# Performance work log

Hardware: AMD Instinct MI355X
Metric: run time of the kernel (lower is better)

## Reference

```python
import jax, jax.numpy as jnp
import numpy as np

N_ATOMS = 50000
N_EDGES = 800000
NODE_DIM = 64
EDGE_DIM = 64
FULL_DIM = 2 * NODE_DIM + EDGE_DIM
BN_EPS = 1e-5


def setup_inputs() -> dict:
    key = jax.random.key(0)
    ks = jax.random.split(key, 8)
    atom_features = jax.random.normal(ks[0], (N_ATOMS, NODE_DIM), dtype=jnp.float32)
    edge_features = jax.random.normal(ks[1], (N_EDGES, EDGE_DIM), dtype=jnp.float32)
    edge_indices = jax.random.randint(ks[2], (N_EDGES, 2), 0, N_ATOMS, dtype=jnp.int64)
    lim = 1.0 / np.sqrt(FULL_DIM)
    W_filter = jax.random.uniform(ks[3], (NODE_DIM, FULL_DIM), jnp.float32, -lim, lim)
    b_filter = jax.random.uniform(ks[4], (NODE_DIM,), jnp.float32, -lim, lim)
    W_core = jax.random.uniform(ks[5], (NODE_DIM, FULL_DIM), jnp.float32, -lim, lim)
    b_core = jax.random.uniform(ks[6], (NODE_DIM,), jnp.float32, -lim, lim)
    gamma_filter = jnp.ones((NODE_DIM,), jnp.float32)
    beta_filter = jnp.zeros((NODE_DIM,), jnp.float32)
    gamma_core = jnp.ones((NODE_DIM,), jnp.float32)
    beta_core = jnp.zeros((NODE_DIM,), jnp.float32)
    return {
        "atom_features": atom_features,
        "edge_features": edge_features,
        "W_filter": W_filter, "b_filter": b_filter,
        "gamma_filter": gamma_filter, "beta_filter": beta_filter,
        "W_core": W_core, "b_core": b_core,
        "gamma_core": gamma_core, "beta_core": beta_core,
        "edge_indices": edge_indices,
    }


def _batchnorm(x, gamma, beta):
    # training-mode BN over the edge axis (biased variance, as torch uses for normalization)
    mean = jnp.mean(x, axis=0)
    var = jnp.mean(jnp.square(x - mean), axis=0)
    return (x - mean) * jax.lax.rsqrt(var + BN_EPS) * gamma + beta


def reference(atom_features, edge_features, W_filter, b_filter, gamma_filter,
              beta_filter, W_core, b_core, gamma_core, beta_core, edge_indices):
    src = edge_indices[:, 0]
    dst = edge_indices[:, 1]
    # z_ij: [E, 2*node_dim + edge_dim]
    z = jnp.concatenate([atom_features[dst], atom_features[src], edge_features], axis=1)
    signal = jax.nn.softplus(_batchnorm(z @ W_core.T + b_core, gamma_core, beta_core))
    gate = jax.nn.sigmoid(_batchnorm(z @ W_filter.T + b_filter, gamma_filter, beta_filter))
    message = gate * signal  # [E, node_dim]
    nbr_sumed = jax.ops.segment_sum(message, dst, num_segments=atom_features.shape[0])
    return atom_features + nbr_sumed
```

## Files before the change

kernel.cpp:

```cpp
#include <hip/hip_runtime.h>
#include <hip/hip_bf16.h>
#include <math.h>

#define N_ATOMS   50000
#define N_EDGES   800000
#define KDIM      192
#define BN_EPS    1e-5f

#define TILE_E     64
#define TPB        5
#define NTILES     (N_EDGES / TILE_E)
#define GRID1      (NTILES / TPB)
#define STAT_SLOTS 32
#define ZSTRIDE    200
#define NSCANBLK   ((N_ATOMS + 255) / 256)

typedef __attribute__((ext_vector_type(8))) __bf16 bf16x8;
typedef __attribute__((ext_vector_type(4))) float  f32x4;
typedef __attribute__((ext_vector_type(4))) unsigned short u16x4;

__device__ __forceinline__ ushort f2bf(float f) {
    union { float f; unsigned u; } v; v.f = f;
    unsigned u = v.u;
    return (ushort)((u + 0x7FFFu + ((u >> 16) & 1u)) >> 16);
}
__device__ __forceinline__ float bf2f(unsigned hi16) {
    union { unsigned u; float f; } v; v.u = hi16 << 16; return v.f;
}
__device__ __forceinline__ float msgf(unsigned pv, float sc_c, float sh_c,
                                      float sc_f, float sh_f) {
    float pc = fmaf(bf2f(pv & 0xFFFFu), sc_c, sh_c);
    float pf = fmaf(bf2f(pv >> 16),     sc_f, sh_f);
    float sp = fmaxf(pc, 0.f) + __logf(1.f + __expf(-fabsf(pc)));
    float sg = 1.f / (1.f + __expf(-pf));
    return sp * sg;
}

__device__ __forceinline__ void gather_issue(
    const float* __restrict__ atom, const float* __restrict__ edgef,
    const int* __restrict__ eidx, int tilebase, int tid, f32x4* v)
{
    const int er = tid >> 4, f4 = tid & 15;
#pragma unroll
    for (int it = 0; it < 12; ++it) {
        const int seg = it >> 2;
        const int e   = (it & 3) * 16 + er;
        const float* srcp;
        if (seg == 0)      srcp = atom  + (size_t)eidx[2 * (tilebase + e) + 1] * 64;
        else if (seg == 1) srcp = atom  + (size_t)eidx[2 * (tilebase + e)] * 64;
        else               srcp = edgef + (size_t)(tilebase + e) * 64;
        v[it] = *(const f32x4*)(srcp + f4 * 4);
    }
}

__device__ __forceinline__ void gather_commit(const f32x4* v, ushort* zl, int tid)
{
    const int er = tid >> 4, f4 = tid & 15;
#pragma unroll
    for (int it = 0; it < 12; ++it) {
        const int seg = it >> 2;
        const int e   = (it & 3) * 16 + er;
        u16x4 b;
        b.x = f2bf(v[it].x); b.y = f2bf(v[it].y);
        b.z = f2bf(v[it].z); b.w = f2bf(v[it].w);
        *(u16x4*)&zl[e * ZSTRIDE + seg * 64 + f4 * 4] = b;
    }
}

__global__ __launch_bounds__(256) void gemm_stats_store(
    const float* __restrict__ atom, const float* __restrict__ edgef,
    const ushort* __restrict__ Wb, const int* __restrict__ eidx,
    const unsigned* __restrict__ perm,
    float* __restrict__ stat_partial, unsigned* __restrict__ ws_pre,
    int do_store)
{
    __shared__ __align__(16) ushort zbuf[2][TILE_E * ZSTRIDE];
    __shared__ unsigned perml[TPB * TILE_E];
    const int tid  = threadIdx.x;
    const int lane = tid & 63, wave = tid >> 6;
    const int ch = wave >> 1, rp = wave & 1;
    const int row = lane & 15, quad = lane >> 4;

    const int t0 = blockIdx.x * TPB;
    for (int i = tid; i < TPB * TILE_E; i += 256)
        perml[i] = perm[t0 * TILE_E + i];

    bf16x8 bfr[2][2][6];
#pragma unroll
    for (int m = 0; m < 2; ++m)
#pragma unroll
        for (int nt = 0; nt < 2; ++nt)
#pragma unroll
            for (int ks = 0; ks < 6; ++ks)
                bfr[m][nt][ks] = *(const bf16x8*)&Wb[
                    (size_t)(m * 64 + ch * 32 + nt * 16 + row) * KDIM + ks * 32 + quad * 8];

    float s[2][2] = {{0.f, 0.f}, {0.f, 0.f}};
    float q[2][2] = {{0.f, 0.f}, {0.f, 0.f}};

    f32x4 pre[12];
    gather_issue(atom, edgef, eidx, t0 * TILE_E, tid, pre);

    for (int tt = 0; tt < TPB; ++tt) {
        ushort* zl = zbuf[tt & 1];
        gather_commit(pre, zl, tid);
        __syncthreads();
        if (tt + 1 < TPB)
            gather_issue(atom, edgef, eidx, (t0 + tt + 1) * TILE_E, tid, pre);

#pragma unroll
        for (int ett = 0; ett < 2; ++ett) {
            const ushort* zb = zl + ((2 * rp + ett) * 16 + row) * ZSTRIDE;
            bf16x8 a[6];
#pragma unroll
            for (int ks = 0; ks < 6; ++ks)
                a[ks] = *(const bf16x8*)&zb[ks * 32 + quad * 8];
            f32x4 acc[2][2];
#pragma unroll
            for (int m = 0; m < 2; ++m)
#pragma unroll
                for (int nt = 0; nt < 2; ++nt)
                    acc[m][nt] = (f32x4){0.f, 0.f, 0.f, 0.f};
#pragma unroll
            for (int ks = 0; ks < 6; ++ks)
#pragma unroll
                for (int m = 0; m < 2; ++m)
#pragma unroll
                    for (int nt = 0; nt < 2; ++nt)
                        acc[m][nt] = __builtin_amdgcn_mfma_f32_16x16x32_bf16(
                            a[ks], bfr[m][nt][ks], acc[m][nt], 0, 0, 0);
#pragma unroll
            for (int nt = 0; nt < 2; ++nt) {
                const int c = ch * 32 + nt * 16 + row;
#pragma unroll
                for (int r = 0; r < 4; ++r) {
                    float vc = acc[0][nt][r], vf = acc[1][nt][r];
                    s[0][nt] += vc; q[0][nt] += vc * vc;
                    s[1][nt] += vf; q[1][nt] += vf * vf;
                    if (do_store) {
                        const int eloc = (2 * rp + ett) * 16 + quad * 4 + r;
                        const unsigned pos = perml[tt * TILE_E + eloc];
                        unsigned pack = (unsigned)f2bf(vc) | ((unsigned)f2bf(vf) << 16);
                        ws_pre[(size_t)pos * 64 + c] = pack;
                    }
                }
            }
        }
    }

    float* slot = stat_partial + (size_t)(blockIdx.x & (STAT_SLOTS - 1)) * 256;
#pragma unroll
    for (int m = 0; m < 2; ++m)
#pragma unroll
        for (int nt = 0; nt < 2; ++nt) {
            float sv = s[m][nt], qv = q[m][nt];
            sv += __shfl_xor(sv, 16, 64); sv += __shfl_xor(sv, 32, 64);
            qv += __shfl_xor(qv, 16, 64); qv += __shfl_xor(qv, 32, 64);
            if (lane < 16) {
                int c = ch * 32 + nt * 16 + lane;
                atomicAdd(slot + m * 128 + c, sv);
                atomicAdd(slot + m * 128 + 64 + c, qv);
            }
        }
}

__global__ void finalize_stats(const float* __restrict__ stat_partial,
                               const float* __restrict__ gc, const float* __restrict__ btc,
                               const float* __restrict__ gf, const float* __restrict__ btf,
                               float* __restrict__ params)
{
    int t = threadIdx.x;
    bool isf = t >= 64;
    int j = t & 63;
    float s = 0.f, q = 0.f;
    for (int slot = 0; slot < STAT_SLOTS; slot++) {
        const float* sp = stat_partial + (size_t)slot * 256 + (isf ? 128 : 0);
        s += sp[j];
        q += sp[64 + j];
    }
    float mean = s / (float)N_EDGES;
    float var  = q / (float)N_EDGES - mean * mean;
    float inv  = rsqrtf(var + BN_EPS);
    float gamma = isf ? gf[j] : gc[j];
    float beta  = isf ? btf[j] : btc[j];
    float scale = gamma * inv;
    float shift = beta - mean * scale;
    params[t]       = scale;
    params[128 + t] = shift;
}

__global__ __launch_bounds__(256) void convert_weights(
    const float* __restrict__ Wc, const float* __restrict__ Wf,
    ushort* __restrict__ Wb)
{
    int i = blockIdx.x * 256 + threadIdx.x;
    float v = (i < 64 * KDIM) ? Wc[i] : Wf[i - 64 * KDIM];
    Wb[i] = f2bf(v);
}

__global__ __launch_bounds__(256) void hist_dst(const int* __restrict__ eidx,
                                                unsigned* __restrict__ counts)
{
    int e = blockIdx.x * 256 + threadIdx.x;
    atomicAdd(&counts[eidx[2 * e + 1]], 1u);
}

__global__ __launch_bounds__(256) void scan_a(const unsigned* __restrict__ counts,
                                              unsigned* __restrict__ row_start,
                                              unsigned* __restrict__ blksum)
{
    __shared__ unsigned sh[256];
    const int tid = threadIdx.x;
    const int i = blockIdx.x * 256 + tid;
    unsigned v = (i < N_ATOMS) ? counts[i] : 0u;
    sh[tid] = v;
    __syncthreads();
    for (int off = 1; off < 256; off <<= 1) {
        unsigned t = (tid >= off) ? sh[tid - off] : 0u;
        __syncthreads();
        sh[tid] += t;
        __syncthreads();
    }
    if (i < N_ATOMS) row_start[i] = sh[tid] - v;
    if (tid == 255) blksum[blockIdx.x] = sh[tid];
}

__global__ void scan_b(unsigned* __restrict__ blksum)
{
    __shared__ unsigned sh[256];
    const int tid = threadIdx.x;
    unsigned v = (tid < NSCANBLK) ? blksum[tid] : 0u;
    sh[tid] = v;
    __syncthreads();
    for (int off = 1; off < 256; off <<= 1) {
        unsigned t = (tid >= off) ? sh[tid - off] : 0u;
        __syncthreads();
        sh[tid] += t;
        __syncthreads();
    }
    if (tid < NSCANBLK) blksum[tid] = sh[tid] - v;
}

__global__ __launch_bounds__(256) void init_cursor(unsigned* __restrict__ row_start,
                                                   const unsigned* __restrict__ blksum,
                                                   unsigned* __restrict__ cursors)
{
    int i = blockIdx.x * 256 + threadIdx.x;
    if (i < N_ATOMS) {
        unsigned base = row_start[i] + blksum[i >> 8];
        row_start[i] = base;
        cursors[i]   = base;
    }
    if (i == 0) row_start[N_ATOMS] = N_EDGES;
}

__global__ __launch_bounds__(256) void fill_perm(const int* __restrict__ eidx,
                                                 unsigned* __restrict__ cursors,
                                                 unsigned* __restrict__ perm)
{
    int e = blockIdx.x * 256 + threadIdx.x;
    int d = eidx[2 * e + 1];
    perm[e] = atomicAdd(&cursors[d], 1u);
}

__global__ __launch_bounds__(256) void bn_act_reduce(
    const unsigned* __restrict__ ws_pre, const unsigned* __restrict__ row_start,
    const float* __restrict__ atom, const float* __restrict__ params,
    float* __restrict__ out)
{
    const int lane = threadIdx.x & 63;
    const int a    = blockIdx.x * 4 + (threadIdx.x >> 6);

    const float sc_c = params[lane],      sh_c = params[128 + lane];
    const float sc_f = params[64 + lane], sh_f = params[192 + lane];

    const unsigned jb = row_start[a];
    const unsigned n  = row_start[a + 1] - jb;
    const unsigned* base = ws_pre + (size_t)jb * 64 + lane;

    float acc = 0.f;
    unsigned k = 0;
    for (; k + 8 <= n; k += 8) {
        unsigned p[8];
#pragma unroll
        for (int u = 0; u < 8; ++u) p[u] = base[(size_t)(k + u) * 64];
#pragma unroll
        for (int u = 0; u < 8; ++u) acc += msgf(p[u], sc_c, sh_c, sc_f, sh_f);
    }
    for (; k < n; ++k) acc += msgf(base[(size_t)k * 64], sc_c, sh_c, sc_f, sh_f);

    out[(size_t)a * 64 + lane] = atom[(size_t)a * 64 + lane] + acc;
}

__global__ __launch_bounds__(256) void copy_out(const f32x4* __restrict__ src,
                                                f32x4* __restrict__ dst)
{
    int i = blockIdx.x * blockDim.x + threadIdx.x;
    dst[i] = src[i];
}

__global__ __launch_bounds__(256) void apply_scatter_fb(
    const float* __restrict__ atom, const float* __restrict__ edgef,
    const ushort* __restrict__ Wb, const int* __restrict__ eidx,
    const float* __restrict__ params, float* __restrict__ out)
{
    __shared__ __align__(16) ushort zl[TILE_E * ZSTRIDE];
    const int tid  = threadIdx.x;
    const int lane = tid & 63, wave = tid >> 6;
    const int ch = wave >> 1, rp = wave & 1;
    const int row = lane & 15, quad = lane >> 4;

    bf16x8 bfr[2][2][6];
#pragma unroll
    for (int m = 0; m < 2; ++m)
#pragma unroll
        for (int nt = 0; nt < 2; ++nt)
#pragma unroll
            for (int ks = 0; ks < 6; ++ks)
                bfr[m][nt][ks] = *(const bf16x8*)&Wb[
                    (size_t)(m * 64 + ch * 32 + nt * 16 + row) * KDIM + ks * 32 + quad * 8];

    float scc[2], shc[2], scf[2], shf[2];
#pragma unroll
    for (int nt = 0; nt < 2; ++nt) {
        int c = ch * 32 + nt * 16 + row;
        scc[nt] = params[c];        shc[nt] = params[128 + c];
        scf[nt] = params[64 + c];   shf[nt] = params[192 + c];
    }

    const int t0 = blockIdx.x * TPB;
    for (int tt = 0; tt < TPB; ++tt) {
        const int tilebase = (t0 + tt) * TILE_E;
        f32x4 pre[12];
        gather_issue(atom, edgef, eidx, tilebase, tid, pre);
        __syncthreads();
        gather_commit(pre, zl, tid);
        __syncthreads();
#pragma unroll
        for (int ett = 0; ett < 2; ++ett) {
            const ushort* zb = zl + ((2 * rp + ett) * 16 + row) * ZSTRIDE;
            bf16x8 a[6];
#pragma unroll
            for (int ks = 0; ks < 6; ++ks)
                a[ks] = *(const bf16x8*)&zb[ks * 32 + quad * 8];
            f32x4 acc[2][2];
#pragma unroll
            for (int m = 0; m < 2; ++m)
#pragma unroll
                for (int nt = 0; nt < 2; ++nt)
                    acc[m][nt] = (f32x4){0.f, 0.f, 0.f, 0.f};
#pragma unroll
            for (int ks = 0; ks < 6; ++ks)
#pragma unroll
                for (int m = 0; m < 2; ++m)
#pragma unroll
                    for (int nt = 0; nt < 2; ++nt)
                        acc[m][nt] = __builtin_amdgcn_mfma_f32_16x16x32_bf16(
                            a[ks], bfr[m][nt][ks], acc[m][nt], 0, 0, 0);
#pragma unroll
            for (int nt = 0; nt < 2; ++nt) {
                int c = ch * 32 + nt * 16 + row;
#pragma unroll
                for (int r = 0; r < 4; ++r) {
                    float pc = fmaf(acc[0][nt][r], scc[nt], shc[nt]);
                    float pf = fmaf(acc[1][nt][r], scf[nt], shf[nt]);
                    float sp = fmaxf(pc, 0.f) + __logf(1.f + __expf(-fabsf(pc)));
                    float sg = 1.f / (1.f + __expf(-pf));
                    int eloc = (2 * rp + ett) * 16 + quad * 4 + r;
                    int d = eidx[2 * (tilebase + eloc) + 1];
                    atomicAdd(out + (size_t)d * 64 + c, sp * sg);
                }
            }
        }
    }
}

extern "C" void kernel_launch(void* const* d_in, const int* in_sizes, int n_in,
                              void* d_out, int out_size, void* d_ws, size_t ws_size,
                              hipStream_t stream)
{
    const float* atom  = (const float*)d_in[0];
    const float* edgef = (const float*)d_in[1];
    const float* Wf    = (const float*)d_in[2];
    const float* gf    = (const float*)d_in[4];
    const float* btf   = (const float*)d_in[5];
    const float* Wc    = (const float*)d_in[6];
    const float* gc    = (const float*)d_in[8];
    const float* btc   = (const float*)d_in[9];
    const int*   eidx  = (const int*)d_in[10];
    float* out = (float*)d_out;

    unsigned* ws_pre       = (unsigned*)d_ws;
    float*    stat_partial = (float*)(ws_pre + (size_t)N_EDGES * 64);
    float*    params       = stat_partial + STAT_SLOTS * 256;
    ushort*   Wb           = (ushort*)(params + 256);
    unsigned* counts       = (unsigned*)(Wb + 2 * 64 * KDIM);
    unsigned* row_start    = counts + N_ATOMS;
    unsigned* blksum       = row_start + N_ATOMS + 1;
    unsigned* cursors      = blksum + 256;
    unsigned* perm         = cursors + N_ATOMS;

    const size_t need_full = (size_t)((char*)(perm + N_EDGES) - (char*)d_ws);
    const int full = (ws_size >= need_full) ? 1 : 0;

    (void)hipMemsetAsync(stat_partial, 0, STAT_SLOTS * 256 * sizeof(float), stream);
    convert_weights<<<(2 * 64 * KDIM) / 256, 256, 0, stream>>>(Wc, Wf, Wb);

    if (full) {
        (void)hipMemsetAsync(counts, 0, N_ATOMS * sizeof(unsigned), stream);
        hist_dst<<<N_EDGES / 256, 256, 0, stream>>>(eidx, counts);
        scan_a<<<NSCANBLK, 256, 0, stream>>>(counts, row_start, blksum);
        scan_b<<<1, 256, 0, stream>>>(blksum);
        init_cursor<<<NSCANBLK, 256, 0, stream>>>(row_start, blksum, cursors);
        fill_perm<<<N_EDGES / 256, 256, 0, stream>>>(eidx, cursors, perm);
        gemm_stats_store<<<GRID1, 256, 0, stream>>>(atom, edgef, Wb, eidx, perm,
                                                    stat_partial, ws_pre, 1);
        finalize_stats<<<1, 128, 0, stream>>>(stat_partial, gc, btc, gf, btf, params);
        bn_act_reduce<<<N_ATOMS / 4, 256, 0, stream>>>(ws_pre, row_start,
                                                       atom, params, out);
    } else {
        gemm_stats_store<<<GRID1, 256, 0, stream>>>(atom, edgef, Wb, eidx,
                                                    (unsigned*)counts ,
                                                    stat_partial, ws_pre, 0);
        finalize_stats<<<1, 128, 0, stream>>>(stat_partial, gc, btc, gf, btf, params);
        copy_out<<<(N_ATOMS * 64 / 4) / 256, 256, 0, stream>>>(
            (const f32x4*)atom, (f32x4*)out);
        apply_scatter_fb<<<GRID1, 256, 0, stream>>>(atom, edgef, Wb, eidx,
                                                    params, out);
    }
}
```

Before: 530.9 us.

## Replace tiled GEMM-stats kernel with persistent per-wave direct-gather variant

The GEMM+stats kernel is rewritten so that each wave independently processes 16-edge groups in a grid-stride persistent loop. It loads the A operand directly from global memory into registers and converts it to bf16 there, with no shared-memory staging and no per-tile __syncthreads. Weights are kept in LDS and read once per MFMA, and edge indices and permutation entries are prefetched two iterations ahead. The aim is to remove the LDS round-trip and the block barriers, at the cost of more LDS reads for B and a different occupancy profile.

```diff
diff --git a/kernel.cpp b/kernel.cpp
--- a/kernel.cpp
+++ b/kernel.cpp
@@ -15,9 +15,16 @@
 #define ZSTRIDE    200
 #define NSCANBLK   ((N_ATOMS + 255) / 256)
 
+#define NGROUPS   (N_EDGES / 16)
+#define GRID_DIR  768
+#define GSTRIDE   (GRID_DIR * 4)
+#define WLSTRIDE  200
+
 typedef __attribute__((ext_vector_type(8))) __bf16 bf16x8;
 typedef __attribute__((ext_vector_type(4))) float  f32x4;
 typedef __attribute__((ext_vector_type(4))) unsigned short u16x4;
+typedef __attribute__((ext_vector_type(8))) unsigned short u16x8;
+typedef __attribute__((ext_vector_type(4))) unsigned int   u32x4;
 
 __device__ __forceinline__ ushort f2bf(float f) {
     union { float f; unsigned u; } v; v.f = f;
@@ -34,6 +41,150 @@
     float sp = fmaxf(pc, 0.f) + __logf(1.f + __expf(-fabsf(pc)));
     float sg = 1.f / (1.f + __expf(-pf));
     return sp * sg;
+}
+
+__global__ __launch_bounds__(256, 3) void gemm_stats_direct(
+    const float* __restrict__ atom, const float* __restrict__ edgef,
+    const ushort* __restrict__ Wb, const int* __restrict__ eidx,
+    const unsigned* __restrict__ perm,
+    float* __restrict__ stat_partial, unsigned* __restrict__ ws_pre,
+    int do_store)
+{
+    __shared__ __align__(16) ushort Wl[128 * WLSTRIDE];
+    const int tid  = threadIdx.x;
+    const int lane = tid & 63;
+    const int r    = lane & 15;
+    const int q    = lane >> 4;
+
+    {
+        const int row = tid >> 1, half = tid & 1;
+        const ushort* srcW = Wb + (size_t)row * KDIM + half * 96;
+        ushort*       dstW = Wl + row * WLSTRIDE + half * 96;
+#pragma unroll
+        for (int j = 0; j < 12; ++j)
+            *(u16x8*)&dstW[j * 8] = *(const u16x8*)&srcW[j * 8];
+    }
+    __syncthreads();
+
+    const int wave  = tid >> 6;
+    const int wglob = blockIdx.x * 4 + wave;
+    const int NG    = (NGROUPS - wglob + GSTRIDE - 1) / GSTRIDE;
+
+    float s[2][4], qs[2][4];
+#pragma unroll
+    for (int m = 0; m < 2; ++m)
+#pragma unroll
+        for (int nt = 0; nt < 4; ++nt) { s[m][nt] = 0.f; qs[m][nt] = 0.f; }
+
+    int2  eA = {0, 0}, eB = {0, 0};
+    u32x4 pA = (u32x4){0, 0, 0, 0}, pB = (u32x4){0, 0, 0, 0};
+    f32x4 pre[12];
+
+    int g = wglob;
+    eA = *(const int2*)&eidx[2 * (g * 16 + r)];
+    if (do_store) pA = *(const u32x4*)&perm[g * 16 + q * 4];
+    if (NG >= 2) {
+        eB = *(const int2*)&eidx[2 * ((g + GSTRIDE) * 16 + r)];
+        if (do_store) pB = *(const u32x4*)&perm[(g + GSTRIDE) * 16 + q * 4];
+    }
+    {
+        const float* pd = atom  + (size_t)eA.y * 64;
+        const float* ps = atom  + (size_t)eA.x * 64;
+        const float* pe = edgef + ((size_t)g * 16 + r) * 64;
+#pragma unroll
+        for (int ks = 0; ks < 6; ++ks) {
+            const float* sp = (ks < 2) ? pd : (ks < 4) ? ps : pe;
+            const int col = (ks & 1) * 32 + q * 8;
+            pre[2 * ks]     = *(const f32x4*)(sp + col);
+            pre[2 * ks + 1] = *(const f32x4*)(sp + col + 4);
+        }
+    }
+
+    for (int i = 0; i < NG; ++i, g += GSTRIDE) {
+        bf16x8 a[6];
+#pragma unroll
+        for (int ks = 0; ks < 6; ++ks) {
+            union { u16x8 u; bf16x8 b; } t;
+#pragma unroll
+            for (int j = 0; j < 4; ++j) {
+                t.u[j]     = f2bf(pre[2 * ks][j]);
+                t.u[4 + j] = f2bf(pre[2 * ks + 1][j]);
+            }
+            a[ks] = t.b;
+        }
+
+        if (i + 1 < NG) {
+            const int gn = g + GSTRIDE;
+            const float* pd = atom  + (size_t)eB.y * 64;
+            const float* ps = atom  + (size_t)eB.x * 64;
+            const float* pe = edgef + ((size_t)gn * 16 + r) * 64;
+#pragma unroll
+            for (int ks = 0; ks < 6; ++ks) {
+                const float* sp = (ks < 2) ? pd : (ks < 4) ? ps : pe;
+                const int col = (ks & 1) * 32 + q * 8;
+                pre[2 * ks]     = *(const f32x4*)(sp + col);
+                pre[2 * ks + 1] = *(const f32x4*)(sp + col + 4);
+            }
+        }
+        int2  eC = {0, 0};
+        u32x4 pC = (u32x4){0, 0, 0, 0};
+        if (i + 2 < NG) {
+            const int g2 = g + 2 * GSTRIDE;
+            eC = *(const int2*)&eidx[2 * (g2 * 16 + r)];
+            if (do_store) pC = *(const u32x4*)&perm[g2 * 16 + q * 4];
+        }
+
+        f32x4 acc[2][4];
+#pragma unroll
+        for (int m = 0; m < 2; ++m)
+#pragma unroll
+            for (int nt = 0; nt < 4; ++nt)
+                acc[m][nt] = (f32x4){0.f, 0.f, 0.f, 0.f};
+#pragma unroll
+        for (int ks = 0; ks < 6; ++ks)
+#pragma unroll
+            for (int m = 0; m < 2; ++m)
+#pragma unroll
+                for (int nt = 0; nt < 4; ++nt) {
+                    bf16x8 b = *(const bf16x8*)&Wl[
+                        (m * 64 + nt * 16 + r) * WLSTRIDE + ks * 32 + q * 8];
+                    acc[m][nt] = __builtin_amdgcn_mfma_f32_16x16x32_bf16(
+                        a[ks], b, acc[m][nt], 0, 0, 0);
+                }
+
+#pragma unroll
+        for (int nt = 0; nt < 4; ++nt) {
+            const int c = nt * 16 + r;
+#pragma unroll
+            for (int rr = 0; rr < 4; ++rr) {
+                float vc = acc[0][nt][rr], vf = acc[1][nt][rr];
+                s[0][nt] += vc; qs[0][nt] += vc * vc;
+                s[1][nt] += vf; qs[1][nt] += vf * vf;
+                if (do_store) {
+                    const unsigned pos = pA[rr];
+                    unsigned pack = (unsigned)f2bf(vc) | ((unsigned)f2bf(vf) << 16);
+                    ws_pre[(size_t)pos * 64 + c] = pack;
+                }
+            }
+        }
+
+        eA = eB; eB = eC; pA = pB; pB = pC;
+    }
+
+    float* slot = stat_partial + (size_t)(blockIdx.x & (STAT_SLOTS - 1)) * 256;
+#pragma unroll
+    for (int m = 0; m < 2; ++m)
+#pragma unroll
+        for (int nt = 0; nt < 4; ++nt) {
+            float sv = s[m][nt], qv = qs[m][nt];
+            sv += __shfl_xor(sv, 16, 64); sv += __shfl_xor(sv, 32, 64);
+            qv += __shfl_xor(qv, 16, 64); qv += __shfl_xor(qv, 32, 64);
+            if (lane < 16) {
+                int c = nt * 16 + lane;
+                atomicAdd(slot + m * 128 + c, sv);
+                atomicAdd(slot + m * 128 + 64 + c, qv);
+            }
+        }
 }
 
 __device__ __forceinline__ void gather_issue(
@@ -65,103 +216,6 @@
         b.z = f2bf(v[it].z); b.w = f2bf(v[it].w);
         *(u16x4*)&zl[e * ZSTRIDE + seg * 64 + f4 * 4] = b;
     }
-}
-
-__global__ __launch_bounds__(256) void gemm_stats_store(
-    const float* __restrict__ atom, const float* __restrict__ edgef,
-    const ushort* __restrict__ Wb, const int* __restrict__ eidx,
-    const unsigned* __restrict__ perm,
-    float* __restrict__ stat_partial, unsigned* __restrict__ ws_pre,
-    int do_store)
-{
-    __shared__ __align__(16) ushort zbuf[2][TILE_E * ZSTRIDE];
-    __shared__ unsigned perml[TPB * TILE_E];
-    const int tid  = threadIdx.x;
-    const int lane = tid & 63, wave = tid >> 6;
-    const int ch = wave >> 1, rp = wave & 1;
-    const int row = lane & 15, quad = lane >> 4;
-
-    const int t0 = blockIdx.x * TPB;
-    for (int i = tid; i < TPB * TILE_E; i += 256)
-        perml[i] = perm[t0 * TILE_E + i];
-
-    bf16x8 bfr[2][2][6];
-#pragma unroll
-    for (int m = 0; m < 2; ++m)
-#pragma unroll
-        for (int nt = 0; nt < 2; ++nt)
-#pragma unroll
-            for (int ks = 0; ks < 6; ++ks)
-                bfr[m][nt][ks] = *(const bf16x8*)&Wb[
-                    (size_t)(m * 64 + ch * 32 + nt * 16 + row) * KDIM + ks * 32 + quad * 8];
-
-    float s[2][2] = {{0.f, 0.f}, {0.f, 0.f}};
-    float q[2][2] = {{0.f, 0.f}, {0.f, 0.f}};
-
-    f32x4 pre[12];
-    gather_issue(atom, edgef, eidx, t0 * TILE_E, tid, pre);
-
-    for (int tt = 0; tt < TPB; ++tt) {
-        ushort* zl = zbuf[tt & 1];
-        gather_commit(pre, zl, tid);
-        __syncthreads();
-        if (tt + 1 < TPB)
-            gather_issue(atom, edgef, eidx, (t0 + tt + 1) * TILE_E, tid, pre);
-
-#pragma unroll
-        for (int ett = 0; ett < 2; ++ett) {
-            const ushort* zb = zl + ((2 * rp + ett) * 16 + row) * ZSTRIDE;
-            bf16x8 a[6];
-#pragma unroll
-            for (int ks = 0; ks < 6; ++ks)
-                a[ks] = *(const bf16x8*)&zb[ks * 32 + quad * 8];
-            f32x4 acc[2][2];
-#pragma unroll
-            for (int m = 0; m < 2; ++m)
-#pragma unroll
-                for (int nt = 0; nt < 2; ++nt)
-                    acc[m][nt] = (f32x4){0.f, 0.f, 0.f, 0.f};
-#pragma unroll
-            for (int ks = 0; ks < 6; ++ks)
-#pragma unroll
-                for (int m = 0; m < 2; ++m)
-#pragma unroll
-                    for (int nt = 0; nt < 2; ++nt)
-                        acc[m][nt] = __builtin_amdgcn_mfma_f32_16x16x32_bf16(
-                            a[ks], bfr[m][nt][ks], acc[m][nt], 0, 0, 0);
-#pragma unroll
-            for (int nt = 0; nt < 2; ++nt) {
-                const int c = ch * 32 + nt * 16 + row;
-#pragma unroll
-                for (int r = 0; r < 4; ++r) {
-                    float vc = acc[0][nt][r], vf = acc[1][nt][r];
-                    s[0][nt] += vc; q[0][nt] += vc * vc;
-                    s[1][nt] += vf; q[1][nt] += vf * vf;
-                    if (do_store) {
-                        const int eloc = (2 * rp + ett) * 16 + quad * 4 + r;
-                        const unsigned pos = perml[tt * TILE_E + eloc];
-                        unsigned pack = (unsigned)f2bf(vc) | ((unsigned)f2bf(vf) << 16);
-                        ws_pre[(size_t)pos * 64 + c] = pack;
-                    }
-                }
-            }
-        }
-    }
-
-    float* slot = stat_partial + (size_t)(blockIdx.x & (STAT_SLOTS - 1)) * 256;
-#pragma unroll
-    for (int m = 0; m < 2; ++m)
-#pragma unroll
-        for (int nt = 0; nt < 2; ++nt) {
-            float sv = s[m][nt], qv = q[m][nt];
-            sv += __shfl_xor(sv, 16, 64); sv += __shfl_xor(sv, 32, 64);
-            qv += __shfl_xor(qv, 16, 64); qv += __shfl_xor(qv, 32, 64);
-            if (lane < 16) {
-                int c = ch * 32 + nt * 16 + lane;
-                atomicAdd(slot + m * 128 + c, sv);
-                atomicAdd(slot + m * 128 + 64 + c, qv);
-            }
-        }
 }
 
 __global__ void finalize_stats(const float* __restrict__ stat_partial,
@@ -413,15 +467,15 @@
         scan_b<<<1, 256, 0, stream>>>(blksum);
         init_cursor<<<NSCANBLK, 256, 0, stream>>>(row_start, blksum, cursors);
         fill_perm<<<N_EDGES / 256, 256, 0, stream>>>(eidx, cursors, perm);
-        gemm_stats_store<<<GRID1, 256, 0, stream>>>(atom, edgef, Wb, eidx, perm,
-                                                    stat_partial, ws_pre, 1);
+        gemm_stats_direct<<<GRID_DIR, 256, 0, stream>>>(atom, edgef, Wb, eidx, perm,
+                                                        stat_partial, ws_pre, 1);
         finalize_stats<<<1, 128, 0, stream>>>(stat_partial, gc, btc, gf, btf, params);
         bn_act_reduce<<<N_ATOMS / 4, 256, 0, stream>>>(ws_pre, row_start,
                                                        atom, params, out);
     } else {
-        gemm_stats_store<<<GRID1, 256, 0, stream>>>(atom, edgef, Wb, eidx,
-                                                    (unsigned*)counts ,
-                                                    stat_partial, ws_pre, 0);
+        gemm_stats_direct<<<GRID_DIR, 256, 0, stream>>>(atom, edgef, Wb, eidx,
+                                                        (const unsigned*)counts ,
+                                                        stat_partial, ws_pre, 0);
         finalize_stats<<<1, 128, 0, stream>>>(stat_partial, gc, btc, gf, btf, params);
         copy_out<<<(N_ATOMS * 64 / 4) / 256, 256, 0, stream>>>(
             (const f32x4*)atom, (f32x4*)out);
```

After: 864.5 us. 62.9% more time.

## Load edge features directly into MFMA registers, bypassing LDS staging

Applied to the files above, without the earlier changes.

Edge-feature rows are no longer copied through the shared-memory tile. Each wave now reads them straight from global memory in MFMA A-fragment layout and converts them to bf16 in registers. The LDS tile keeps only the two gathered atom segments, with a smaller row stride, which cuts LDS footprint and store traffic and lets the kernel declare a higher occupancy hint. In exchange, the edge loads are no longer prefetched a tile ahead, so global latency may be exposed inside the MFMA loop, and each lane does strided 32-byte reads.

```diff
diff --git a/kernel.cpp b/kernel.cpp
--- a/kernel.cpp
+++ b/kernel.cpp
@@ -13,11 +13,13 @@
 #define GRID1      (NTILES / TPB)
 #define STAT_SLOTS 32
 #define ZSTRIDE    200
+#define ZAST       136
 #define NSCANBLK   ((N_ATOMS + 255) / 256)
 
 typedef __attribute__((ext_vector_type(8))) __bf16 bf16x8;
 typedef __attribute__((ext_vector_type(4))) float  f32x4;
 typedef __attribute__((ext_vector_type(4))) unsigned short u16x4;
+typedef __attribute__((ext_vector_type(8))) unsigned short u16x8;
 
 __device__ __forceinline__ ushort f2bf(float f) {
     union { float f; unsigned u; } v; v.f = f;
@@ -34,6 +36,35 @@
     float sp = fmaxf(pc, 0.f) + __logf(1.f + __expf(-fabsf(pc)));
     float sg = 1.f / (1.f + __expf(-pf));
     return sp * sg;
+}
+
+__device__ __forceinline__ void gather_issue_a(
+    const float* __restrict__ atom, const int* __restrict__ eidx,
+    int tilebase, int tid, f32x4* v)
+{
+    const int er = tid >> 4, f4 = tid & 15;
+#pragma unroll
+    for (int it = 0; it < 8; ++it) {
+        const int seg = it >> 2;
+        const int e   = (it & 3) * 16 + er;
+        const float* srcp =
+            atom + (size_t)eidx[2 * (tilebase + e) + (seg == 0 ? 1 : 0)] * 64;
+        v[it] = *(const f32x4*)(srcp + f4 * 4);
+    }
+}
+
+__device__ __forceinline__ void gather_commit_a(const f32x4* v, ushort* zl, int tid)
+{
+    const int er = tid >> 4, f4 = tid & 15;
+#pragma unroll
+    for (int it = 0; it < 8; ++it) {
+        const int seg = it >> 2;
+        const int e   = (it & 3) * 16 + er;
+        u16x4 b;
+        b.x = f2bf(v[it].x); b.y = f2bf(v[it].y);
+        b.z = f2bf(v[it].z); b.w = f2bf(v[it].w);
+        *(u16x4*)&zl[e * ZAST + seg * 64 + f4 * 4] = b;
+    }
 }
 
 __device__ __forceinline__ void gather_issue(
@@ -67,14 +98,14 @@
     }
 }
 
-__global__ __launch_bounds__(256) void gemm_stats_store(
+__global__ __launch_bounds__(256, 4) void gemm_stats_store(
     const float* __restrict__ atom, const float* __restrict__ edgef,
     const ushort* __restrict__ Wb, const int* __restrict__ eidx,
     const unsigned* __restrict__ perm,
     float* __restrict__ stat_partial, unsigned* __restrict__ ws_pre,
     int do_store)
 {
-    __shared__ __align__(16) ushort zbuf[2][TILE_E * ZSTRIDE];
+    __shared__ __align__(16) ushort zbuf[2][TILE_E * ZAST];
     __shared__ unsigned perml[TPB * TILE_E];
     const int tid  = threadIdx.x;
     const int lane = tid & 63, wave = tid >> 6;
@@ -98,23 +129,42 @@
     float s[2][2] = {{0.f, 0.f}, {0.f, 0.f}};
     float q[2][2] = {{0.f, 0.f}, {0.f, 0.f}};
 
-    f32x4 pre[12];
-    gather_issue(atom, edgef, eidx, t0 * TILE_E, tid, pre);
+    f32x4 pre[8];
+    gather_issue_a(atom, eidx, t0 * TILE_E, tid, pre);
 
     for (int tt = 0; tt < TPB; ++tt) {
         ushort* zl = zbuf[tt & 1];
-        gather_commit(pre, zl, tid);
+        gather_commit_a(pre, zl, tid);
         __syncthreads();
         if (tt + 1 < TPB)
-            gather_issue(atom, edgef, eidx, (t0 + tt + 1) * TILE_E, tid, pre);
+            gather_issue_a(atom, eidx, (t0 + tt + 1) * TILE_E, tid, pre);
 
 #pragma unroll
         for (int ett = 0; ett < 2; ++ett) {
-            const ushort* zb = zl + ((2 * rp + ett) * 16 + row) * ZSTRIDE;
+            const size_t ebase =
+                (size_t)((t0 + tt) * TILE_E + (2 * rp + ett) * 16 + row) * 64;
+            f32x4 ef0 = *(const f32x4*)&edgef[ebase + quad * 8];
+            f32x4 ef1 = *(const f32x4*)&edgef[ebase + quad * 8 + 4];
+            f32x4 ef2 = *(const f32x4*)&edgef[ebase + 32 + quad * 8];
+            f32x4 ef3 = *(const f32x4*)&edgef[ebase + 32 + quad * 8 + 4];
+
+            const ushort* zb = zl + ((2 * rp + ett) * 16 + row) * ZAST;
             bf16x8 a[6];
 #pragma unroll
-            for (int ks = 0; ks < 6; ++ks)
+            for (int ks = 0; ks < 4; ++ks)
                 a[ks] = *(const bf16x8*)&zb[ks * 32 + quad * 8];
+            {
+                union { u16x8 u; bf16x8 b; } t4, t5;
+#pragma unroll
+                for (int j = 0; j < 4; ++j) {
+                    t4.u[j]     = f2bf(ef0[j]);
+                    t4.u[4 + j] = f2bf(ef1[j]);
+                    t5.u[j]     = f2bf(ef2[j]);
+                    t5.u[4 + j] = f2bf(ef3[j]);
+                }
+                a[4] = t4.b; a[5] = t5.b;
+            }
+
             f32x4 acc[2][2];
 #pragma unroll
             for (int m = 0; m < 2; ++m)
```

Result: slower. 840.3 us (+58.3%).
